# Kernel optimization log

Hardware: AMD Instinct MI355X
Metric: run time of the kernel (lower is better)

## Reference

```python
import jax, jax.numpy as jnp
import numpy as np

NUM_HEADS = 8
SCALE = 25.0
SIM_THRESH = 0.75


def setup_inputs() -> dict:
    key = jax.random.key(0)
    ks = jax.random.split(key, 6)
    B, N, C = 1, 2048, 1024
    x_cls = jax.random.normal(ks[0], (B, N, C), jnp.float32)
    x_reg = jax.random.normal(ks[1], (B, N, C), jnp.float32)
    cls_score = jax.random.uniform(ks[2], (N,), jnp.float32)
    fg_score = jax.random.uniform(ks[3], (N,), jnp.float32)
    W_qkv_cls = jax.random.normal(ks[4], (3 * C, C), jnp.float32) * 0.02
    W_qkv_reg = jax.random.normal(ks[5], (3 * C, C), jnp.float32) * 0.02
    return {"x_cls": x_cls, "x_reg": x_reg, "cls_score": cls_score,
            "fg_score": fg_score, "W_qkv_cls": W_qkv_cls, "W_qkv_reg": W_qkv_reg}


def _l2norm(t):
    return t / jnp.linalg.norm(t, axis=-1, keepdims=True)


def reference(x_cls, x_reg, cls_score, fg_score, W_qkv_cls, W_qkv_reg):
    B, N, C = x_cls.shape
    H = NUM_HEADS
    d = C // H

    def qkv(x, W):
        # (B,N,3C) -> (3,B,H,N,d)
        t = (x @ W.T).reshape(B, N, 3, H, d).transpose(2, 0, 3, 1, 4)
        return t[0], t[1], t[2]

    q_cls, k_cls, v_cls = qkv(x_cls, W_qkv_cls)
    q_reg, k_reg, _ = qkv(x_reg, W_qkv_reg)

    q_cls, k_cls = _l2norm(q_cls), _l2norm(k_cls)
    q_reg, k_reg = _l2norm(q_reg), _l2norm(k_reg)
    v_cls_normed = _l2norm(v_cls)

    # scores broadcast: s[..., i, j] = score[j]; transpose -> score[i]
    s_cls = cls_score.reshape(1, 1, 1, N)
    s_fg = fg_score.reshape(1, 1, 1, N)
    # use_mask=True branch
    m_cls = (s_cls > jnp.swapaxes(s_cls, -2, -1) - 0.1).astype(x_cls.dtype)
    m_fg = (s_fg > jnp.swapaxes(s_fg, -2, -1) - 0.1).astype(x_cls.dtype)

    attn_cls_raw = jnp.einsum('bhid,bhjd->bhij', v_cls_normed, v_cls_normed)

    attn_cls = jax.nn.softmax(
        jnp.einsum('bhid,bhjd->bhij', q_cls, k_cls) * SCALE * s_cls * m_cls, axis=-1)
    attn_reg = jax.nn.softmax(
        jnp.einsum('bhid,bhjd->bhij', q_reg, k_reg) * SCALE * s_fg * m_fg, axis=-1)
    attn = (attn_reg + attn_cls) * 0.5

    x = jnp.einsum('bhij,bhjd->bhid', attn, v_cls).transpose(0, 2, 1, 3).reshape(B, N, C)
    x_ori = v_cls.transpose(0, 2, 1, 3).reshape(B, N, C)
    x_out = jnp.concatenate([x, x_ori], axis=-1)  # (B, N, 2C)

    # ave=True branch (batch 0, head-mean)
    raw = attn_cls_raw.sum(axis=1)[0] / H  # (N, N)
    sim_mask = (raw > SIM_THRESH).astype(x_cls.dtype)
    sim_attn = attn.sum(axis=1)[0] / H
    sim_round2 = jax.nn.softmax(sim_attn, axis=-1)
    sim_round2 = sim_mask * sim_round2
    sim_round2 = sim_round2 / jnp.sum(sim_round2, axis=-1, keepdims=True)
    return x_out, sim_round2
```

## Files before the change

### kernel.cpp

```cpp
#include <hip/hip_runtime.h>


#define NTOK 2048
#define CDIM 1024
#define OD   5120

typedef __attribute__((ext_vector_type(8))) short bf16x8;
typedef __attribute__((ext_vector_type(4))) short s16x4;
typedef __attribute__((ext_vector_type(2))) short s16x2;
typedef __attribute__((ext_vector_type(4))) float f32x4;

#define MFMA16(a,b,c) __builtin_amdgcn_mfma_f32_16x16x32_bf16((a),(b),(c),0,0,0)

__device__ __forceinline__ short f2bf(float x){
  unsigned u = __float_as_uint(x);
  u += 0x7FFFu + ((u >> 16) & 1u);
  return (short)(u >> 16);
}

__device__ __forceinline__ int cvtpk(float lo, float hi){
  int r;
  asm("v_cvt_pk_bf16_f32 %0, %1, %2" : "=v"(r) : "v"(lo), "v"(hi));
  return r;
}

__device__ __forceinline__ void atomAddF(float* p, float v){
  unsafeAtomicAdd(p, v);
}

__device__ __forceinline__ void gld16(const short* g, short* l){
  __builtin_amdgcn_global_load_lds(
      (const __attribute__((address_space(1))) unsigned int*)g,
      (__attribute__((address_space(3))) unsigned int*)l, 16, 0, 0);
}

__global__ __launch_bounds__(256,8) void k_cvt(
    const float* __restrict__ xc, const float* __restrict__ xr,
    const float* __restrict__ Wc, const float* __restrict__ Wr,
    short* __restrict__ xbc, short* __restrict__ xbr,
    short* __restrict__ wbc, short* __restrict__ wbr)
{
  int idx = blockIdx.x*256 + threadIdx.x;
  const float* src; short* dst; int off;
  if      (idx <  262144){ src = xc; dst = xbc; off = idx; }
  else if (idx <  524288){ src = xr; dst = xbr; off = idx - 262144; }
  else if (idx <  917504){ src = Wc; dst = wbc; off = idx - 524288; }
  else                   { src = Wr; dst = wbr; off = idx - 917504; }
  float4 a = *(const float4*)(src + (size_t)off*8);
  float4 b = *(const float4*)(src + (size_t)off*8 + 4);
  bf16x8 o = { f2bf(a.x), f2bf(a.y), f2bf(a.z), f2bf(a.w),
               f2bf(b.x), f2bf(b.y), f2bf(b.z), f2bf(b.w) };
  *(bf16x8*)(dst + (size_t)off*8) = o;
}

__global__ __launch_bounds__(256,3) void k_qkv(
    const short* __restrict__ xbc, const short* __restrict__ xbr,
    const short* __restrict__ wbc, const short* __restrict__ wbr,
    float* __restrict__ tmp)
{
  const int tid = threadIdx.x;
  const int l   = tid & 63;
  const int w   = tid >> 6;
  const int fr  = l & 15;
  const int fk8 = (l >> 4) * 8;

  const int L     = blockIdx.x;
  const int xcd   = L & 7;
  const int slot  = L >> 3;
  const int panel = xcd*5 + (slot >> 4);
  const int mb    = slot & 15;
  const int m0    = mb * 128;
  const int o0    = panel * 128;

  const short* Xb; const short* Wb; int wrow;
  if (o0 < 3072){ Xb = xbc; Wb = wbc; wrow = o0; }
  else          { Xb = xbr; Wb = wbr; wrow = o0 - 3072; }

  __shared__ __align__(16) short Ab[2][8][64][8];
  __shared__ __align__(16) short Bb[2][8][64][8];

  const int wr = w >> 1;
  const int wc = w & 1;

#define QSTAGE(DB, KN) do {                                                  \
    _Pragma("unroll")                                                        \
    for (int it=0; it<2; ++it){                                              \
      int f = it*4 + w;                                                      \
      gld16(Xb + (size_t)(m0  + f*16 + fr)*CDIM + (KN) + fk8,                \
            &Ab[DB][f][0][0]);                                               \
      gld16(Wb + (size_t)(wrow + f*16 + fr)*CDIM + (KN) + fk8,               \
            &Bb[DB][f][0][0]);                                               \
    }                                                                        \
  } while(0)

  f32x4 acc[4][4] = {};

  QSTAGE(0, 0);
  __syncthreads();

  for (int kt = 0; kt < 32; ++kt){
    const int db = kt & 1;
    if (kt < 31){ if (db) QSTAGE(0, (kt+1)*32); else QSTAGE(1, (kt+1)*32); }
    bf16x8 af[4], bfr[4];
    #pragma unroll
    for (int ai=0;ai<4;ai++) af[ai]  = *(const bf16x8*)&Ab[db][wr*4+ai][l][0];
    #pragma unroll
    for (int bj=0;bj<4;bj++) bfr[bj] = *(const bf16x8*)&Bb[db][wc*4+bj][l][0];
    #pragma unroll
    for (int ai=0;ai<4;ai++)
      #pragma unroll
      for (int bj=0;bj<4;bj++)
        acc[ai][bj] = MFMA16(af[ai], bfr[bj], acc[ai][bj]);
    __syncthreads();
  }
#undef QSTAGE

  #pragma unroll
  for (int ai=0;ai<4;ai++)
    #pragma unroll
    for (int bj=0;bj<4;bj++)
      #pragma unroll
      for (int r=0;r<4;r++)
        tmp[(size_t)(m0 + wr*64 + ai*16 + (l>>4)*4 + r)*OD
            + o0 + wc*64 + bj*16 + fr] = acc[ai][bj][r];
}

__global__ __launch_bounds__(256,4) void k_norm(
    const float* __restrict__ tmp, float* __restrict__ out,
    short* __restrict__ qc, short* __restrict__ kc,
    short* __restrict__ qr, short* __restrict__ kr,
    short* __restrict__ vn, short* __restrict__ vb)
{
  int task = blockIdx.x*4 + (threadIdx.x>>6);
  int lane = threadIdx.x & 63;
  int n = task / 40;
  int rem = task - n*40;
  int chunk = rem >> 3;
  int h = rem & 7;
  const float* src = tmp + (size_t)n*OD + (chunk<<10) + h*128;
  float2 v = *(const float2*)(src + lane*2);
  float ss = v.x*v.x + v.y*v.y;
  #pragma unroll
  for (int m=1;m<64;m<<=1) ss += __shfl_xor(ss, m);
  float rn = 1.0f / sqrtf(ss);
  size_t base = ((size_t)h*NTOK + n)*128 + lane*2;
  s16x2 nv = { f2bf(v.x*rn), f2bf(v.y*rn) };
  switch(chunk){
    case 0: *(s16x2*)&qc[base] = nv; break;
    case 1: *(s16x2*)&kc[base] = nv; break;
    case 3: *(s16x2*)&qr[base] = nv; break;
    case 4: *(s16x2*)&kr[base] = nv; break;
    default: {
      *(s16x2*)&vn[base] = nv;
      *(s16x2*)&vb[base] = (s16x2){ f2bf(v.x), f2bf(v.y) };
      *(float2*)&out[(size_t)n*2048 + 1024 + h*128 + lane*2] = v;
      break;
    }
  }
}

__global__ __launch_bounds__(256,4) void k_vT(
    const short* __restrict__ vb, short* __restrict__ vT)
{
  int b = blockIdx.x;
  int h  = b >> 6;
  int nt = (b >> 1) & 31;
  int dt = b & 1;
  __shared__ short t[64][72];
  int tid = threadIdx.x;
  int r  = tid >> 2;
  int c0 = (tid & 3) << 4;
  #pragma unroll
  for (int u=0;u<2;u++){
    bf16x8 val = *(const bf16x8*)&vb[((size_t)h*NTOK + nt*64 + r)*128 + dt*64 + c0 + u*8];
    #pragma unroll
    for (int e=0;e<8;e++) t[r][c0+u*8+e] = val[e];
  }
  __syncthreads();
  #pragma unroll
  for (int u=0;u<2;u++){
    bf16x8 o;
    #pragma unroll
    for (int e=0;e<8;e++) o[e] = t[c0+u*8+e][r];
    *(bf16x8*)&vT[((size_t)h*128 + dt*64 + r)*NTOK + nt*64 + c0 + u*8] = o;
  }
}

#define JLEN 1024

__global__ __launch_bounds__(256,2) void k_attn(
    const short* __restrict__ qc, const short* __restrict__ kc,
    const short* __restrict__ qr, const short* __restrict__ kr,
    const short* __restrict__ vT,
    const float* __restrict__ csc, const float* __restrict__ fsc,
    float* __restrict__ s_cls, float* __restrict__ s_reg,
    float* __restrict__ Up)
{
  const int tid = threadIdx.x;
  const int l   = tid & 63;
  const int w   = tid >> 6;
  const int L    = blockIdx.x;
  const int xcd  = L & 7;
  const int slot = L >> 3;
  const int hs   = ((slot >> 5) << 3) | xcd;
  const int h    = hs >> 1;
  const int s    = hs & 1;
  const int rem  = slot & 31;
  const int js   = rem >> 4;
  const int ib   = rem & 15;

  const int iw  = ib * 128 + w * 32;
  const int fr  = l & 15;
  const int g   = l >> 4;
  const int fk8 = g * 8;
  const size_t hN = (size_t)h * NTOK;
  const size_t hD = (size_t)h * 128;

  const short* Qp = s ? qr : qc;
  const short* Kp = s ? kr : kc;
  const float* sc = s ? fsc : csc;
  float* ssum     = s ? s_reg : s_cls;
  float* Ub       = Up + (size_t)(js*2 + s) * 2097152;

  __shared__ __align__(16) short Kbuf[2][4][4][64][8];
  __shared__ __align__(16) short Vbuf[2][8][2][64][8];

  const int t8 = w * 8;

#define STAGE(DB, JN) do {                                                   \
    _Pragma("unroll")                                                        \
    for (int q8=0; q8<8; ++q8){                                              \
      int t = t8 + q8;                                                       \
      if (t < 16){                                                           \
        int jf = t >> 2, kk = t & 3;                                         \
        gld16(Kp + (hN + (JN) + jf*16 + fr)*128 + kk*32 + fk8,               \
              &Kbuf[DB][jf][kk][0][0]);                                      \
      } else {                                                               \
        int u = t - 16, df = u >> 1, ks = u & 1;                             \
        gld16(vT + (hD + df*16 + fr)*2048 + (JN) + ks*32 + fk8,              \
              &Vbuf[DB][df][ks][0][0]);                                      \
      }                                                                      \
    }                                                                        \
  } while(0)

  bf16x8 bq[2][4];
  #pragma unroll
  for (int i2=0;i2<2;i2++)
    #pragma unroll
    for (int kk=0;kk<4;kk++)
      bq[i2][kk] = *(const bf16x8*)&Qp[(hN + iw + i2*16 + fr)*128 + kk*32 + fk8];

  float sci[2];
  sci[0] = sc[iw + fr] - 0.1f;
  sci[1] = sc[iw + 16 + fr] - 0.1f;

  f32x4 U[2][8] = {};
  float p[2] = {0.f, 0.f};

  const int srcA = ((((g<<1)    & 3) << 4) + fr) << 2;
  const int srcB = ((((g<<1 | 1)& 3) << 4) + fr) << 2;
  const bool ghi = g >= 2;
  const int jbase = js * JLEN;

  STAGE(0, jbase);
  __syncthreads();

  for (int jt = 0; jt < 16; ++jt){
    const int db = jt & 1;
    const int j0 = jbase + jt*64;
    if (jt < 15){ if (db) STAGE(0, j0 + 64); else STAGE(1, j0 + 64); }
    #pragma unroll
    for (int ks=0; ks<2; ++ks){
      int cpk[2][2][2];
      #pragma unroll
      for (int t=0; t<2; ++t){
        const int jf = ks*2 + t;
        f32x4 S0 = {}; f32x4 S1 = {};
        __builtin_amdgcn_s_setprio(1);
        #pragma unroll
        for (int kk=0; kk<4; ++kk){
          bf16x8 kb = *(const bf16x8*)&Kbuf[db][jf][kk][l][0];
          S0 = MFMA16(kb, bq[0][kk], S0);
          S1 = MFMA16(kb, bq[1][kk], S1);
        }
        __builtin_amdgcn_s_setprio(0);
        float4 sjv = *(const float4*)&sc[j0 + jf*16 + 4*g];
        float e0[4], e1[4];
        #pragma unroll
        for (int r=0;r<4;r++){
          float sj = (&sjv.x)[r];
          float sj25 = 25.0f * sj;
          e0[r] = (sj > sci[0]) ? __expf(S0[r]*sj25) : 1.0f;
          e1[r] = (sj > sci[1]) ? __expf(S1[r]*sj25) : 1.0f;
          p[0] += e0[r]; p[1] += e1[r];
        }
        cpk[0][t][0] = cvtpk(e0[0], e0[1]);
        cpk[0][t][1] = cvtpk(e0[2], e0[3]);
        cpk[1][t][0] = cvtpk(e1[0], e1[1]);
        cpk[1][t][1] = cvtpk(e1[2], e1[3]);
      }
      bf16x8 ea[2];
      #pragma unroll
      for (int i2=0;i2<2;i2++){
        int a0 = __builtin_amdgcn_ds_bpermute(srcA, cpk[i2][0][0]);
        int a1 = __builtin_amdgcn_ds_bpermute(srcA, cpk[i2][0][1]);
        int a2 = __builtin_amdgcn_ds_bpermute(srcA, cpk[i2][1][0]);
        int a3 = __builtin_amdgcn_ds_bpermute(srcA, cpk[i2][1][1]);
        int b0 = __builtin_amdgcn_ds_bpermute(srcB, cpk[i2][0][0]);
        int b1 = __builtin_amdgcn_ds_bpermute(srcB, cpk[i2][0][1]);
        int b2 = __builtin_amdgcn_ds_bpermute(srcB, cpk[i2][1][0]);
        int b3 = __builtin_amdgcn_ds_bpermute(srcB, cpk[i2][1][1]);
        int wd[4];
        wd[0] = ghi ? a2 : a0;  wd[1] = ghi ? a3 : a1;
        wd[2] = ghi ? b2 : b0;  wd[3] = ghi ? b3 : b1;
        ea[i2] = *(bf16x8*)wd;
      }
      __builtin_amdgcn_s_setprio(1);
      #pragma unroll
      for (int df=0; df<8; ++df){
        bf16x8 bv = *(const bf16x8*)&Vbuf[db][df][ks][l][0];
        U[0][df] = MFMA16(ea[0], bv, U[0][df]);
        U[1][df] = MFMA16(ea[1], bv, U[1][df]);
      }
      __builtin_amdgcn_s_setprio(0);
    }
    __syncthreads();
  }
#undef STAGE

  #pragma unroll
  for (int i2=0;i2<2;i2++){
    p[i2] += __shfl_xor(p[i2], 16);
    p[i2] += __shfl_xor(p[i2], 32);
  }
  if (l < 16){
    atomAddF(&ssum[hN + iw + l],      p[0]);
    atomAddF(&ssum[hN + iw + 16 + l], p[1]);
  }
  #pragma unroll
  for (int i2=0;i2<2;i2++)
    #pragma unroll
    for (int df=0;df<8;df++)
      #pragma unroll
      for (int r=0;r<4;r++)
        Ub[(hN + iw + i2*16 + g*4 + r)*128 + df*16 + fr] = U[i2][df][r];
}

__global__ __launch_bounds__(256,8) void k_attn_fin(
    const float* __restrict__ Up,
    const float* __restrict__ s_cls, const float* __restrict__ s_reg,
    float* __restrict__ out)
{
  int task = blockIdx.x*4 + (threadIdx.x>>6);
  int lane = threadIdx.x & 63;
  int h = task >> 11;
  int row = task & 2047;
  size_t b = (size_t)task*128 + lane*2;
  float2 c0 = *(const float2*)(Up + 0*2097152 + b);
  float2 r0 = *(const float2*)(Up + 1*2097152 + b);
  float2 c1 = *(const float2*)(Up + 2*2097152 + b);
  float2 r1 = *(const float2*)(Up + 3*2097152 + b);
  float isc = 0.5f/s_cls[task];
  float isr = 0.5f/s_reg[task];
  float2 o = { (c0.x+c1.x)*isc + (r0.x+r1.x)*isr,
               (c0.y+c1.y)*isc + (r0.y+r1.y)*isr };
  *(float2*)&out[(size_t)row*2048 + h*128 + lane*2] = o;
}

__global__ __launch_bounds__(256,2) void k_sim(
    const short* __restrict__ qc, const short* __restrict__ kc,
    const short* __restrict__ qr, const short* __restrict__ kr,
    const float* __restrict__ csc, const float* __restrict__ fsc,
    const float* __restrict__ s_cls, const float* __restrict__ s_reg,
    float* __restrict__ out)
{
  const int tid  = threadIdx.x;
  const int lane = tid & 63;
  const int w    = tid >> 6;
  const int i0w  = blockIdx.x * 128 + w * 32;
  const int j0   = blockIdx.y * 64;
  const int fr   = lane & 15;
  const int fk   = (lane >> 4) * 8;

  __shared__ __align__(16) short Bsh[2][16][64][8];

  float sjc[4], sjf[4];
  #pragma unroll
  for (int js=0;js<4;js++){ sjc[js]=csc[j0+js*16+fr]; sjf[js]=fsc[j0+js*16+fr]; }
  int rowb[2]; float sci[2][4], sfi[2][4];
  #pragma unroll
  for (int ri=0;ri<2;ri++){
    rowb[ri] = i0w + ri*16 + ((lane>>4)<<2);
    #pragma unroll
    for (int r=0;r<4;r++){ sci[ri][r]=csc[rowb[ri]+r]; sfi[ri][r]=fsc[rowb[ri]+r]; }
  }

  f32x4 sim[2][4] = {};

  for (int h=0; h<8; ++h){
    const size_t hb = (size_t)h * NTOK;
    bf16x8 aq[2][4], ar[2][4];
    #pragma unroll
    for (int ri=0;ri<2;ri++)
      #pragma unroll
      for (int kk=0;kk<4;kk++){
        aq[ri][kk] = *(const bf16x8*)&qc[(hb + i0w + ri*16 + fr)*128 + kk*32 + fk];
        ar[ri][kk] = *(const bf16x8*)&qr[(hb + i0w + ri*16 + fr)*128 + kk*32 + fk];
      }
    float iscl[2][4], isrl[2][4];
    #pragma unroll
    for (int ri=0;ri<2;ri++)
      #pragma unroll
      for (int r=0;r<4;r++){
        iscl[ri][r] = 1.0f/s_cls[hb + rowb[ri] + r];
        isrl[ri][r] = 1.0f/s_reg[hb + rowb[ri] + r];
      }
    __syncthreads();
    #pragma unroll
    for (int it=0; it<8; ++it){
      int slot = it*256 + tid;
      int str  = slot >> 10;
      int frag = (slot >> 6) & 15;
      int l    = slot & 63;
      int r    = (frag >> 2)*16 + (l & 15);
      int c    = (frag & 3)*32 + (l >> 4)*8;
      const short* gp = (str ? kr : kc) + (hb + j0 + r)*128 + c;
      *(bf16x8*)&Bsh[str][frag][l][0] = *(const bf16x8*)gp;
    }
    __syncthreads();
    #pragma unroll
    for (int js=0; js<4; ++js){
      bf16x8 bc[4], br[4];
      #pragma unroll
      for (int kk=0;kk<4;kk++){
        bc[kk] = *(const bf16x8*)&Bsh[0][js*4+kk][lane][0];
        br[kk] = *(const bf16x8*)&Bsh[1][js*4+kk][lane][0];
      }
      #pragma unroll
      for (int ri=0;ri<2;ri++){
        f32x4 Sc = {}; f32x4 Sr = {};
        #pragma unroll
        for (int kk=0;kk<4;kk++){
          Sc = MFMA16(aq[ri][kk], bc[kk], Sc);
          Sr = MFMA16(ar[ri][kk], br[kk], Sr);
        }
        #pragma unroll
        for (int r=0;r<4;r++){
          float ec = (sjc[js] > sci[ri][r]-0.1f) ? __expf(Sc[r]*(25.0f*sjc[js])) : 1.0f;
          float er = (sjf[js] > sfi[ri][r]-0.1f) ? __expf(Sr[r]*(25.0f*sjf[js])) : 1.0f;
          sim[ri][js][r] += ec*iscl[ri][r] + er*isrl[ri][r];
        }
      }
    }
  }
  #pragma unroll
  for (int ri=0;ri<2;ri++)
    #pragma unroll
    for (int js=0;js<4;js++)
      #pragma unroll
      for (int r=0;r<4;r++)
        out[4194304ull + (size_t)(rowb[ri]+r)*2048 + j0 + js*16 + fr]
            = sim[ri][js][r] * 0.0625f;
}

__global__ __launch_bounds__(256,4) void k_raw(
    const short* __restrict__ vn, unsigned char* __restrict__ mask)
{
  const int tid  = threadIdx.x;
  const int lane = tid & 63;
  const int w    = tid >> 6;
  const int i0w  = blockIdx.x * 128 + w * 32;
  const int j0   = blockIdx.y * 64;
  const int fr   = lane & 15;
  const int fk   = (lane >> 4) * 8;

  __shared__ __align__(16) short Bsh[16][64][8];

  f32x4 raw[2][4] = {};

  for (int cc=0; cc<8; ++cc){
    const size_t hb = (size_t)cc * NTOK;
    bf16x8 av[2][4];
    #pragma unroll
    for (int ri=0;ri<2;ri++)
      #pragma unroll
      for (int kk=0;kk<4;kk++)
        av[ri][kk] = *(const bf16x8*)&vn[(hb + i0w + ri*16 + fr)*128 + kk*32 + fk];
    __syncthreads();
    #pragma unroll
    for (int it=0; it<4; ++it){
      int slot = it*256 + tid;
      int frag = (slot >> 6) & 15;
      int l    = slot & 63;
      int r    = (frag >> 2)*16 + (l & 15);
      int c    = (frag & 3)*32 + (l >> 4)*8;
      *(bf16x8*)&Bsh[frag][l][0] = *(const bf16x8*)&vn[(hb + j0 + r)*128 + c];
    }
    __syncthreads();
    #pragma unroll
    for (int js=0; js<4; ++js){
      bf16x8 bv[4];
      #pragma unroll
      for (int kk=0;kk<4;kk++) bv[kk] = *(const bf16x8*)&Bsh[js*4+kk][lane][0];
      #pragma unroll
      for (int ri=0;ri<2;ri++)
        #pragma unroll
        for (int kk=0;kk<4;kk++)
          raw[ri][js] = MFMA16(av[ri][kk], bv[kk], raw[ri][js]);
    }
  }
  const int rb0 = i0w + ((lane>>4)<<2);
  #pragma unroll
  for (int ri=0;ri<2;ri++)
    #pragma unroll
    for (int js=0;js<4;js++)
      #pragma unroll
      for (int r=0;r<4;r++)
        mask[(size_t)(rb0 + ri*16 + r)*2048 + j0 + js*16 + fr]
            = raw[ri][js][r] > 6.0f ? 1 : 0;
}

__global__ __launch_bounds__(256,4) void k_final(
    float* __restrict__ out, const unsigned char* __restrict__ mask)
{
  int row  = blockIdx.x*4 + (threadIdx.x>>6);
  int lane = threadIdx.x & 63;
  float* sr = out + 4194304ull + (size_t)row*2048;
  const unsigned char* mr = mask + (size_t)row*2048;
  float v[32];
  float sum2 = 0.0f;
  #pragma unroll
  for (int c=0;c<32;c++){
    float e = __expf(sr[c*64 + lane]);
    v[c] = (mr[c*64 + lane] != 0) ? e : 0.0f;
    sum2 += v[c];
  }
  #pragma unroll
  for (int m=1;m<64;m<<=1) sum2 += __shfl_xor(sum2, m);
  float inv = 1.0f / sum2;
  #pragma unroll
  for (int c=0;c<32;c++) sr[c*64 + lane] = v[c]*inv;
}

extern "C" void kernel_launch(void* const* d_in, const int* in_sizes, int n_in,
                              void* d_out, int out_size, void* d_ws, size_t ws_size,
                              hipStream_t stream)
{
  const float* xcls = (const float*)d_in[0];
  const float* xreg = (const float*)d_in[1];
  const float* csc  = (const float*)d_in[2];
  const float* fsc  = (const float*)d_in[3];
  const float* Wc   = (const float*)d_in[4];
  const float* Wr   = (const float*)d_in[5];
  float* out = (float*)d_out;

  char* ws = (char*)d_ws;
  float* tmp          = (float*)ws;
  unsigned char* mask = (unsigned char*)ws;
  char* accbase       = ws + 4u*1024*1024;
  float* s_cls        = (float*)(accbase);
  float* s_reg        = (float*)(accbase + 65536);
  float* Up           = (float*)(accbase + 131072);
  short* qc = (short*)(ws + 41943040ull);
  short* kc = qc + 2097152;
  short* qr = kc + 2097152;
  short* kr = qr + 2097152;
  short* vn = kr + 2097152;
  short* vb = vn + 2097152;
  short* vT = vb + 2097152;
  short* xbc = (short*)(ws + 41943040ull);
  short* xbr = xbc + 2097152;
  short* wbc = xbr + 2097152;
  short* wbr = wbc + 3145728;

  k_cvt  <<<4608,        256, 0, stream>>>(xcls, xreg, Wc, Wr, xbc, xbr, wbc, wbr);
  k_qkv  <<<640,         256, 0, stream>>>(xbc, xbr, wbc, wbr, tmp);
  k_norm <<<20480,       256, 0, stream>>>(tmp, out, qc, kc, qr, kr, vn, vb);
  k_vT   <<<512,         256, 0, stream>>>(vb, vT);
  hipMemsetAsync(accbase, 0, 131072, stream);
  k_attn <<<512,         256, 0, stream>>>(qc, kc, qr, kr, vT, csc, fsc,
                                           s_cls, s_reg, Up);
  k_attn_fin <<<4096,    256, 0, stream>>>(Up, s_cls, s_reg, out);
  k_raw  <<<dim3(16,32), 256, 0, stream>>>(vn, mask);
  k_sim  <<<dim3(16,32), 256, 0, stream>>>(qc, kc, qr, kr, csc, fsc, s_cls, s_reg, out);
  k_final<<<512,         256, 0, stream>>>(out, mask);
}
```

Before: 259.2 us.

## Split attention key range four ways with smaller tiles and bf16 partials

The attention kernel now splits the key dimension into four 512-wide chunks instead of two 1024-wide ones. The grid doubles to 1024 blocks, each j-tile shrinks to 32 keys, and shared memory is halved, with launch bounds raised to allow 4 blocks per CU. Partial PV accumulators are stored as bf16 instead of fp32, and the finalize kernel sums four partials per stream. The aim is better occupancy and parallelism in the attention kernel. In exchange, the output loses some precision from bf16 partials, the per-iteration MFMA work is smaller relative to sync overhead, and the workspace holds more partials.

```diff
diff --git a/kernel.cpp b/kernel.cpp
--- a/kernel.cpp
+++ b/kernel.cpp
@@ -16,6 +16,10 @@
   unsigned u = __float_as_uint(x);
   u += 0x7FFFu + ((u >> 16) & 1u);
   return (short)(u >> 16);
+}
+
+__device__ __forceinline__ float bf2f(short s){
+  return __uint_as_float(((unsigned)(unsigned short)s) << 16);
 }
 
 __device__ __forceinline__ int cvtpk(float lo, float hi){
@@ -186,15 +190,15 @@
   }
 }
 
-#define JLEN 1024
-
-__global__ __launch_bounds__(256,2) void k_attn(
+#define JLEN 512
+
+__global__ __launch_bounds__(256,4) void k_attn(
     const short* __restrict__ qc, const short* __restrict__ kc,
     const short* __restrict__ qr, const short* __restrict__ kr,
     const short* __restrict__ vT,
     const float* __restrict__ csc, const float* __restrict__ fsc,
     float* __restrict__ s_cls, float* __restrict__ s_reg,
-    float* __restrict__ Up)
+    short* __restrict__ Up)
 {
   const int tid = threadIdx.x;
   const int l   = tid & 63;
@@ -202,10 +206,10 @@
   const int L    = blockIdx.x;
   const int xcd  = L & 7;
   const int slot = L >> 3;
-  const int hs   = ((slot >> 5) << 3) | xcd;
+  const int hs   = ((slot >> 6) << 3) | xcd;
   const int h    = hs >> 1;
   const int s    = hs & 1;
-  const int rem  = slot & 31;
+  const int rem  = slot & 63;
   const int js   = rem >> 4;
   const int ib   = rem & 15;
 
@@ -220,25 +224,25 @@
   const short* Kp = s ? kr : kc;
   const float* sc = s ? fsc : csc;
   float* ssum     = s ? s_reg : s_cls;
-  float* Ub       = Up + (size_t)(js*2 + s) * 2097152;
-
-  __shared__ __align__(16) short Kbuf[2][4][4][64][8];
-  __shared__ __align__(16) short Vbuf[2][8][2][64][8];
-
-  const int t8 = w * 8;
+  short* Ub       = Up + (size_t)(js*2 + s) * 2097152;
+
+  __shared__ __align__(16) short Kbuf[2][2][4][64][8];
+  __shared__ __align__(16) short Vbuf[2][8][64][8];
+
+  const int t4 = w * 4;
 
 #define STAGE(DB, JN) do {                                                   \
     _Pragma("unroll")                                                        \
-    for (int q8=0; q8<8; ++q8){                                              \
-      int t = t8 + q8;                                                       \
-      if (t < 16){                                                           \
+    for (int q4=0; q4<4; ++q4){                                              \
+      int t = t4 + q4;                                                       \
+      if (t < 8){                                                            \
         int jf = t >> 2, kk = t & 3;                                         \
         gld16(Kp + (hN + (JN) + jf*16 + fr)*128 + kk*32 + fk8,               \
               &Kbuf[DB][jf][kk][0][0]);                                      \
       } else {                                                               \
-        int u = t - 16, df = u >> 1, ks = u & 1;                             \
-        gld16(vT + (hD + df*16 + fr)*2048 + (JN) + ks*32 + fk8,              \
-              &Vbuf[DB][df][ks][0][0]);                                      \
+        int df = t - 8;                                                      \
+        gld16(vT + (hD + df*16 + fr)*2048 + (JN) + fk8,                      \
+              &Vbuf[DB][df][0][0]);                                          \
       }                                                                      \
     }                                                                        \
   } while(0)
@@ -267,63 +271,59 @@
 
   for (int jt = 0; jt < 16; ++jt){
     const int db = jt & 1;
-    const int j0 = jbase + jt*64;
-    if (jt < 15){ if (db) STAGE(0, j0 + 64); else STAGE(1, j0 + 64); }
-    #pragma unroll
-    for (int ks=0; ks<2; ++ks){
-      int cpk[2][2][2];
-      #pragma unroll
-      for (int t=0; t<2; ++t){
-        const int jf = ks*2 + t;
-        f32x4 S0 = {}; f32x4 S1 = {};
-        __builtin_amdgcn_s_setprio(1);
-        #pragma unroll
-        for (int kk=0; kk<4; ++kk){
-          bf16x8 kb = *(const bf16x8*)&Kbuf[db][jf][kk][l][0];
-          S0 = MFMA16(kb, bq[0][kk], S0);
-          S1 = MFMA16(kb, bq[1][kk], S1);
-        }
-        __builtin_amdgcn_s_setprio(0);
-        float4 sjv = *(const float4*)&sc[j0 + jf*16 + 4*g];
-        float e0[4], e1[4];
-        #pragma unroll
-        for (int r=0;r<4;r++){
-          float sj = (&sjv.x)[r];
-          float sj25 = 25.0f * sj;
-          e0[r] = (sj > sci[0]) ? __expf(S0[r]*sj25) : 1.0f;
-          e1[r] = (sj > sci[1]) ? __expf(S1[r]*sj25) : 1.0f;
-          p[0] += e0[r]; p[1] += e1[r];
-        }
-        cpk[0][t][0] = cvtpk(e0[0], e0[1]);
-        cpk[0][t][1] = cvtpk(e0[2], e0[3]);
-        cpk[1][t][0] = cvtpk(e1[0], e1[1]);
-        cpk[1][t][1] = cvtpk(e1[2], e1[3]);
-      }
-      bf16x8 ea[2];
-      #pragma unroll
-      for (int i2=0;i2<2;i2++){
-        int a0 = __builtin_amdgcn_ds_bpermute(srcA, cpk[i2][0][0]);
-        int a1 = __builtin_amdgcn_ds_bpermute(srcA, cpk[i2][0][1]);
-        int a2 = __builtin_amdgcn_ds_bpermute(srcA, cpk[i2][1][0]);
-        int a3 = __builtin_amdgcn_ds_bpermute(srcA, cpk[i2][1][1]);
-        int b0 = __builtin_amdgcn_ds_bpermute(srcB, cpk[i2][0][0]);
-        int b1 = __builtin_amdgcn_ds_bpermute(srcB, cpk[i2][0][1]);
-        int b2 = __builtin_amdgcn_ds_bpermute(srcB, cpk[i2][1][0]);
-        int b3 = __builtin_amdgcn_ds_bpermute(srcB, cpk[i2][1][1]);
-        int wd[4];
-        wd[0] = ghi ? a2 : a0;  wd[1] = ghi ? a3 : a1;
-        wd[2] = ghi ? b2 : b0;  wd[3] = ghi ? b3 : b1;
-        ea[i2] = *(bf16x8*)wd;
-      }
+    const int j0 = jbase + jt*32;
+    if (jt < 15){ if (db) STAGE(0, j0 + 32); else STAGE(1, j0 + 32); }
+    int cpk[2][2][2];
+    #pragma unroll
+    for (int t=0; t<2; ++t){
+      f32x4 S0 = {}; f32x4 S1 = {};
       __builtin_amdgcn_s_setprio(1);
       #pragma unroll
-      for (int df=0; df<8; ++df){
-        bf16x8 bv = *(const bf16x8*)&Vbuf[db][df][ks][l][0];
-        U[0][df] = MFMA16(ea[0], bv, U[0][df]);
-        U[1][df] = MFMA16(ea[1], bv, U[1][df]);
+      for (int kk=0; kk<4; ++kk){
+        bf16x8 kb = *(const bf16x8*)&Kbuf[db][t][kk][l][0];
+        S0 = MFMA16(kb, bq[0][kk], S0);
+        S1 = MFMA16(kb, bq[1][kk], S1);
       }
       __builtin_amdgcn_s_setprio(0);
-    }
+      float4 sjv = *(const float4*)&sc[j0 + t*16 + 4*g];
+      float e0[4], e1[4];
+      #pragma unroll
+      for (int r=0;r<4;r++){
+        float sj = (&sjv.x)[r];
+        float sj25 = 25.0f * sj;
+        e0[r] = (sj > sci[0]) ? __expf(S0[r]*sj25) : 1.0f;
+        e1[r] = (sj > sci[1]) ? __expf(S1[r]*sj25) : 1.0f;
+        p[0] += e0[r]; p[1] += e1[r];
+      }
+      cpk[0][t][0] = cvtpk(e0[0], e0[1]);
+      cpk[0][t][1] = cvtpk(e0[2], e0[3]);
+      cpk[1][t][0] = cvtpk(e1[0], e1[1]);
+      cpk[1][t][1] = cvtpk(e1[2], e1[3]);
+    }
+    bf16x8 ea[2];
+    #pragma unroll
+    for (int i2=0;i2<2;i2++){
+      int a0 = __builtin_amdgcn_ds_bpermute(srcA, cpk[i2][0][0]);
+      int a1 = __builtin_amdgcn_ds_bpermute(srcA, cpk[i2][0][1]);
+      int a2 = __builtin_amdgcn_ds_bpermute(srcA, cpk[i2][1][0]);
+      int a3 = __builtin_amdgcn_ds_bpermute(srcA, cpk[i2][1][1]);
+      int b0 = __builtin_amdgcn_ds_bpermute(srcB, cpk[i2][0][0]);
+      int b1 = __builtin_amdgcn_ds_bpermute(srcB, cpk[i2][0][1]);
+      int b2 = __builtin_amdgcn_ds_bpermute(srcB, cpk[i2][1][0]);
+      int b3 = __builtin_amdgcn_ds_bpermute(srcB, cpk[i2][1][1]);
+      int wd[4];
+      wd[0] = ghi ? a2 : a0;  wd[1] = ghi ? a3 : a1;
+      wd[2] = ghi ? b2 : b0;  wd[3] = ghi ? b3 : b1;
+      ea[i2] = *(bf16x8*)wd;
+    }
+    __builtin_amdgcn_s_setprio(1);
+    #pragma unroll
+    for (int df=0; df<8; ++df){
+      bf16x8 bv = *(const bf16x8*)&Vbuf[db][df][l][0];
+      U[0][df] = MFMA16(ea[0], bv, U[0][df]);
+      U[1][df] = MFMA16(ea[1], bv, U[1][df]);
+    }
+    __builtin_amdgcn_s_setprio(0);
     __syncthreads();
   }
 #undef STAGE
@@ -343,11 +343,11 @@
     for (int df=0;df<8;df++)
       #pragma unroll
       for (int r=0;r<4;r++)
-        Ub[(hN + iw + i2*16 + g*4 + r)*128 + df*16 + fr] = U[i2][df][r];
+        Ub[(hN + iw + i2*16 + g*4 + r)*128 + df*16 + fr] = f2bf(U[i2][df][r]);
 }
 
 __global__ __launch_bounds__(256,8) void k_attn_fin(
-    const float* __restrict__ Up,
+    const short* __restrict__ Up,
     const float* __restrict__ s_cls, const float* __restrict__ s_reg,
     float* __restrict__ out)
 {
@@ -356,14 +356,17 @@
   int h = task >> 11;
   int row = task & 2047;
   size_t b = (size_t)task*128 + lane*2;
-  float2 c0 = *(const float2*)(Up + 0*2097152 + b);
-  float2 r0 = *(const float2*)(Up + 1*2097152 + b);
-  float2 c1 = *(const float2*)(Up + 2*2097152 + b);
-  float2 r1 = *(const float2*)(Up + 3*2097152 + b);
+  float cx=0.f, cy=0.f, rx=0.f, ry=0.f;
+  #pragma unroll
+  for (int js=0; js<4; ++js){
+    s16x2 c = *(const s16x2*)(Up + (size_t)(js*2+0)*2097152 + b);
+    s16x2 r = *(const s16x2*)(Up + (size_t)(js*2+1)*2097152 + b);
+    cx += bf2f(c[0]); cy += bf2f(c[1]);
+    rx += bf2f(r[0]); ry += bf2f(r[1]);
+  }
   float isc = 0.5f/s_cls[task];
   float isr = 0.5f/s_reg[task];
-  float2 o = { (c0.x+c1.x)*isc + (r0.x+r1.x)*isr,
-               (c0.y+c1.y)*isc + (r0.y+r1.y)*isr };
+  float2 o = { cx*isc + rx*isr, cy*isc + ry*isr };
   *(float2*)&out[(size_t)row*2048 + h*128 + lane*2] = o;
 }
 
@@ -560,7 +563,7 @@
   char* accbase       = ws + 4u*1024*1024;
   float* s_cls        = (float*)(accbase);
   float* s_reg        = (float*)(accbase + 65536);
-  float* Up           = (float*)(accbase + 131072);
+  short* Up           = (short*)(accbase + 131072);
   short* qc = (short*)(ws + 41943040ull);
   short* kc = qc + 2097152;
   short* qr = kc + 2097152;
@@ -578,7 +581,7 @@
   k_norm <<<20480,       256, 0, stream>>>(tmp, out, qc, kc, qr, kr, vn, vb);
   k_vT   <<<512,         256, 0, stream>>>(vb, vT);
   hipMemsetAsync(accbase, 0, 131072, stream);
-  k_attn <<<512,         256, 0, stream>>>(qc, kc, qr, kr, vT, csc, fsc,
+  k_attn <<<1024,        256, 0, stream>>>(qc, kc, qr, kr, vT, csc, fsc,
                                            s_cls, s_reg, Up);
   k_attn_fin <<<4096,    256, 0, stream>>>(Up, s_cls, s_reg, out);
   k_raw  <<<dim3(16,32), 256, 0, stream>>>(vn, mask);
```

Result: slower. 337.6 us (+30.3%).

## Fuse L2 normalization into QKV GEMM epilogue and store attention partials in bf16

Applied to the files above, without the earlier changes.

The QKV GEMM epilogue now computes per-row squared norms across the 128-wide head tile using shuffles and a small shared buffer. It then writes normalized bf16 q/k/v and the fp32 v output directly. This removes the fp32 tmp buffer round trip and the separate k_norm launch. Separately, k_attn's partial U outputs are stored as bf16 instead of fp32, halving that traffic at some precision cost. The x/W bf16 buffers are relocated to the workspace start to avoid overlapping the q/k outputs, but they now share that region with the mask and with accbase, which the later memset overwrites.

```diff
diff --git a/kernel.cpp b/kernel.cpp
--- a/kernel.cpp
+++ b/kernel.cpp
@@ -3,7 +3,6 @@
 
 #define NTOK 2048
 #define CDIM 1024
-#define OD   5120
 
 typedef __attribute__((ext_vector_type(8))) short bf16x8;
 typedef __attribute__((ext_vector_type(4))) short s16x4;
@@ -16,6 +15,10 @@
   unsigned u = __float_as_uint(x);
   u += 0x7FFFu + ((u >> 16) & 1u);
   return (short)(u >> 16);
+}
+
+__device__ __forceinline__ float bf2f(short s){
+  return __uint_as_float(((unsigned)(unsigned short)s) << 16);
 }
 
 __device__ __forceinline__ int cvtpk(float lo, float hi){
@@ -56,13 +59,17 @@
 __global__ __launch_bounds__(256,3) void k_qkv(
     const short* __restrict__ xbc, const short* __restrict__ xbr,
     const short* __restrict__ wbc, const short* __restrict__ wbr,
-    float* __restrict__ tmp)
+    short* __restrict__ qc, short* __restrict__ kc,
+    short* __restrict__ qr, short* __restrict__ kr,
+    short* __restrict__ vn, short* __restrict__ vb,
+    float* __restrict__ out)
 {
   const int tid = threadIdx.x;
   const int l   = tid & 63;
   const int w   = tid >> 6;
   const int fr  = l & 15;
-  const int fk8 = (l >> 4) * 8;
+  const int g   = l >> 4;
+  const int fk8 = g * 8;
 
   const int L     = blockIdx.x;
   const int xcd   = L & 7;
@@ -78,6 +85,7 @@
 
   __shared__ __align__(16) short Ab[2][8][64][8];
   __shared__ __align__(16) short Bb[2][8][64][8];
+  __shared__ float nbuf[128][2];
 
   const int wr = w >> 1;
   const int wc = w & 1;
@@ -115,48 +123,55 @@
   }
 #undef QSTAGE
 
+  const int chunk = o0 >> 10;
+  const int hh    = (o0 >> 7) & 7;
+
+  float rn[4][4];
   #pragma unroll
   for (int ai=0;ai<4;ai++)
     #pragma unroll
-    for (int bj=0;bj<4;bj++)
-      #pragma unroll
-      for (int r=0;r<4;r++)
-        tmp[(size_t)(m0 + wr*64 + ai*16 + (l>>4)*4 + r)*OD
-            + o0 + wc*64 + bj*16 + fr] = acc[ai][bj][r];
-}
-
-__global__ __launch_bounds__(256,4) void k_norm(
-    const float* __restrict__ tmp, float* __restrict__ out,
-    short* __restrict__ qc, short* __restrict__ kc,
-    short* __restrict__ qr, short* __restrict__ kr,
-    short* __restrict__ vn, short* __restrict__ vb)
-{
-  int task = blockIdx.x*4 + (threadIdx.x>>6);
-  int lane = threadIdx.x & 63;
-  int n = task / 40;
-  int rem = task - n*40;
-  int chunk = rem >> 3;
-  int h = rem & 7;
-  const float* src = tmp + (size_t)n*OD + (chunk<<10) + h*128;
-  float2 v = *(const float2*)(src + lane*2);
-  float ss = v.x*v.x + v.y*v.y;
-  #pragma unroll
-  for (int m=1;m<64;m<<=1) ss += __shfl_xor(ss, m);
-  float rn = 1.0f / sqrtf(ss);
-  size_t base = ((size_t)h*NTOK + n)*128 + lane*2;
-  s16x2 nv = { f2bf(v.x*rn), f2bf(v.y*rn) };
-  switch(chunk){
-    case 0: *(s16x2*)&qc[base] = nv; break;
-    case 1: *(s16x2*)&kc[base] = nv; break;
-    case 3: *(s16x2*)&qr[base] = nv; break;
-    case 4: *(s16x2*)&kr[base] = nv; break;
-    default: {
-      *(s16x2*)&vn[base] = nv;
-      *(s16x2*)&vb[base] = (s16x2){ f2bf(v.x), f2bf(v.y) };
-      *(float2*)&out[(size_t)n*2048 + 1024 + h*128 + lane*2] = v;
-      break;
-    }
-  }
+    for (int r=0;r<4;r++){
+      float ss = 0.f;
+      #pragma unroll
+      for (int bj=0;bj<4;bj++) ss += acc[ai][bj][r]*acc[ai][bj][r];
+      ss += __shfl_xor(ss, 1); ss += __shfl_xor(ss, 2);
+      ss += __shfl_xor(ss, 4); ss += __shfl_xor(ss, 8);
+      if (fr == 0) nbuf[wr*64 + ai*16 + g*4 + r][wc] = ss;
+      rn[ai][r] = ss;
+    }
+  __syncthreads();
+  #pragma unroll
+  for (int ai=0;ai<4;ai++)
+    #pragma unroll
+    for (int r=0;r<4;r++){
+      int row = wr*64 + ai*16 + g*4 + r;
+      rn[ai][r] = rsqrtf(nbuf[row][0] + nbuf[row][1]);
+    }
+
+  #pragma unroll
+  for (int ai=0;ai<4;ai++)
+    #pragma unroll
+    for (int r=0;r<4;r++){
+      int n   = m0 + wr*64 + ai*16 + g*4 + r;
+      size_t base = ((size_t)hh*NTOK + n)*128;
+      #pragma unroll
+      for (int bj=0;bj<4;bj++){
+        int col = wc*64 + bj*16 + fr;
+        float val = acc[ai][bj][r];
+        short nv  = f2bf(val * rn[ai][r]);
+        switch(chunk){
+          case 0: qc[base+col] = nv; break;
+          case 1: kc[base+col] = nv; break;
+          case 3: qr[base+col] = nv; break;
+          case 4: kr[base+col] = nv; break;
+          default:
+            vn[base+col] = nv;
+            vb[base+col] = f2bf(val);
+            out[(size_t)n*2048 + 1024 + hh*128 + col] = val;
+            break;
+        }
+      }
+    }
 }
 
 __global__ __launch_bounds__(256,4) void k_vT(
@@ -194,7 +209,7 @@
     const short* __restrict__ vT,
     const float* __restrict__ csc, const float* __restrict__ fsc,
     float* __restrict__ s_cls, float* __restrict__ s_reg,
-    float* __restrict__ Up)
+    short* __restrict__ Up)
 {
   const int tid = threadIdx.x;
   const int l   = tid & 63;
@@ -220,7 +235,7 @@
   const short* Kp = s ? kr : kc;
   const float* sc = s ? fsc : csc;
   float* ssum     = s ? s_reg : s_cls;
-  float* Ub       = Up + (size_t)(js*2 + s) * 2097152;
+  short* Ub       = Up + (size_t)(js*2 + s) * 2097152;
 
   __shared__ __align__(16) short Kbuf[2][4][4][64][8];
   __shared__ __align__(16) short Vbuf[2][8][2][64][8];
@@ -343,11 +358,11 @@
     for (int df=0;df<8;df++)
       #pragma unroll
       for (int r=0;r<4;r++)
-        Ub[(hN + iw + i2*16 + g*4 + r)*128 + df*16 + fr] = U[i2][df][r];
+        Ub[(hN + iw + i2*16 + g*4 + r)*128 + df*16 + fr] = f2bf(U[i2][df][r]);
 }
 
 __global__ __launch_bounds__(256,8) void k_attn_fin(
-    const float* __restrict__ Up,
+    const short* __restrict__ Up,
     const float* __restrict__ s_cls, const float* __restrict__ s_reg,
     float* __restrict__ out)
 {
@@ -356,14 +371,17 @@
   int h = task >> 11;
   int row = task & 2047;
   size_t b = (size_t)task*128 + lane*2;
-  float2 c0 = *(const float2*)(Up + 0*2097152 + b);
-  float2 r0 = *(const float2*)(Up + 1*2097152 + b);
-  float2 c1 = *(const float2*)(Up + 2*2097152 + b);
-  float2 r1 = *(const float2*)(Up + 3*2097152 + b);
+  float cx=0.f, cy=0.f, rx=0.f, ry=0.f;
+  #pragma unroll
+  for (int js=0; js<2; ++js){
+    s16x2 c = *(const s16x2*)(Up + (size_t)(js*2+0)*2097152 + b);
+    s16x2 r = *(const s16x2*)(Up + (size_t)(js*2+1)*2097152 + b);
+    cx += bf2f(c[0]); cy += bf2f(c[1]);
+    rx += bf2f(r[0]); ry += bf2f(r[1]);
+  }
   float isc = 0.5f/s_cls[task];
   float isr = 0.5f/s_reg[task];
-  float2 o = { (c0.x+c1.x)*isc + (r0.x+r1.x)*isr,
-               (c0.y+c1.y)*isc + (r0.y+r1.y)*isr };
+  float2 o = { cx*isc + rx*isr, cy*isc + ry*isr };
   *(float2*)&out[(size_t)row*2048 + h*128 + lane*2] = o;
 }
 
@@ -555,12 +573,15 @@
   float* out = (float*)d_out;
 
   char* ws = (char*)d_ws;
-  float* tmp          = (float*)ws;
+  short* xbc = (short*)ws;
+  short* xbr = xbc + 2097152;
+  short* wbc = xbr + 2097152;
+  short* wbr = wbc + 3145728;
   unsigned char* mask = (unsigned char*)ws;
   char* accbase       = ws + 4u*1024*1024;
   float* s_cls        = (float*)(accbase);
   float* s_reg        = (float*)(accbase + 65536);
-  float* Up           = (float*)(accbase + 131072);
+  short* Up           = (short*)(accbase + 131072);
   short* qc = (short*)(ws + 41943040ull);
   short* kc = qc + 2097152;
   short* qr = kc + 2097152;
@@ -568,14 +589,10 @@
   short* vn = kr + 2097152;
   short* vb = vn + 2097152;
   short* vT = vb + 2097152;
-  short* xbc = (short*)(ws + 41943040ull);
-  short* xbr = xbc + 2097152;
-  short* wbc = xbr + 2097152;
-  short* wbr = wbc + 3145728;
 
   k_cvt  <<<4608,        256, 0, stream>>>(xcls, xreg, Wc, Wr, xbc, xbr, wbc, wbr);
-  k_qkv  <<<640,         256, 0, stream>>>(xbc, xbr, wbc, wbr, tmp);
-  k_norm <<<20480,       256, 0, stream>>>(tmp, out, qc, kc, qr, kr, vn, vb);
+  k_qkv  <<<640,         256, 0, stream>>>(xbc, xbr, wbc, wbr,
+                                           qc, kc, qr, kr, vn, vb, out);
   k_vT   <<<512,         256, 0, stream>>>(vb, vT);
   hipMemsetAsync(accbase, 0, 131072, stream);
   k_attn <<<512,         256, 0, stream>>>(qc, kc, qr, kr, vT, csc, fsc,
```

New measurement: 250.0 us. -3.6%, faster.
